# Kernel optimization log

Measured on AMD Instinct MI355X. Metric: run time of the kernel, lower is better.

Reference implementation:

```python
import jax, jax.numpy as jnp
import numpy as np

V, E, HID, T = 50000, 300, 256, 9
B, S = 32, 512
H = HID // 2  # per-direction LSTM hidden


def _lstm_dir(x, wih, whh, bih, bhh, reverse):
    # x: [B,S,D]; torch nn.LSTM gate order: i, f, g, o
    bsz = x.shape[0]
    hdim = whh.shape[1]
    xg = jnp.einsum('bsd,gd->bsg', x, wih) + bih + bhh  # [B,S,4H] precomputed input gates

    def step(carry, xt):
        h, c = carry
        g = xt + h @ whh.T
        i, f, gg, o = jnp.split(g, 4, axis=-1)
        c = jax.nn.sigmoid(f) * c + jax.nn.sigmoid(i) * jnp.tanh(gg)
        h = jax.nn.sigmoid(o) * jnp.tanh(c)
        return (h, c), h

    init = (jnp.zeros((bsz, hdim), x.dtype), jnp.zeros((bsz, hdim), x.dtype))
    _, hs = jax.lax.scan(step, init, jnp.swapaxes(xg, 0, 1), reverse=reverse)
    return jnp.swapaxes(hs, 0, 1)  # [B,S,H]


def _crf_nll(emissions, tags, mask, start_t, end_t, trans_t):
    # pytorch-crf: loss = -mean_b llh, llh = numerator - log-partition
    maskf = mask.astype(emissions.dtype)
    em_tag = jnp.take_along_axis(emissions, tags[..., None], axis=2)[..., 0]  # [B,S]
    trans_sc = trans_t[tags[:, :-1], tags[:, 1:]]  # [B,S-1]
    num = start_t[tags[:, 0]] + em_tag[:, 0] + jnp.sum((trans_sc + em_tag[:, 1:]) * maskf[:, 1:], axis=1)
    seq_len = mask.sum(axis=1)
    last_tags = jnp.take_along_axis(tags, (seq_len - 1)[:, None], axis=1)[:, 0]
    num = num + end_t[last_tags]

    def step(alpha, inp):
        em_t, m_t = inp  # [B,T], [B]
        new = jax.nn.logsumexp(alpha[:, :, None] + trans_t[None] + em_t[:, None, :], axis=1)
        return jnp.where(m_t[:, None], new, alpha), None

    alpha0 = start_t[None] + emissions[:, 0]
    alpha, _ = jax.lax.scan(step, alpha0, (jnp.swapaxes(emissions[:, 1:], 0, 1), jnp.swapaxes(mask[:, 1:], 0, 1)))
    denom = jax.nn.logsumexp(alpha + end_t[None], axis=1)
    return -(num - denom).mean()


def _forward(emb, wih0f, whh0f, bih0f, bhh0f, wih0b, whh0b, bih0b, bhh0b,
             wih1f, whh1f, bih1f, bhh1f, wih1b, whh1b, bih1b, bhh1b,
             wproj, bproj, start_t, end_t, trans_t, x, tags, mask):
    e = emb[x]  # [B,S,E]; dropout is identity in eval mode
    h0 = jnp.concatenate([_lstm_dir(e, wih0f, whh0f, bih0f, bhh0f, False),
                          _lstm_dir(e, wih0b, whh0b, bih0b, bhh0b, True)], axis=-1)
    h1 = jnp.concatenate([_lstm_dir(h0, wih1f, whh1f, bih1f, bhh1f, False),
                          _lstm_dir(h0, wih1b, whh1b, bih1b, bhh1b, True)], axis=-1)
    emissions = jnp.einsum('bsh,th->bst', h1, wproj) + bproj  # [B,S,T]
    return _crf_nll(emissions, tags, mask, start_t, end_t, trans_t)


def setup_inputs() -> dict:
    key = jax.random.key(0)
    ks = jax.random.split(key, 32)

    def n(k, shape, s=0.1):
        return jax.random.normal(k, shape, jnp.float32) * s

    d = {}
    d['emb'] = n(ks[0], (V, E)).at[0].set(0.0)  # padding_idx=0 row zeroed
    i = 1
    for l, din in enumerate([E, HID]):
        for dr in 'fb':
            d['wih%d%s' % (l, dr)] = n(ks[i], (4 * H, din)); i += 1
            d['whh%d%s' % (l, dr)] = n(ks[i], (4 * H, H)); i += 1
            d['bih%d%s' % (l, dr)] = n(ks[i], (4 * H,)); i += 1
            d['bhh%d%s' % (l, dr)] = n(ks[i], (4 * H,)); i += 1
    d['wproj'] = n(ks[i], (T, HID)); i += 1
    d['bproj'] = n(ks[i], (T,)); i += 1
    d['start_t'] = n(ks[i], (T,)); i += 1
    d['end_t'] = n(ks[i], (T,)); i += 1
    d['trans_t'] = n(ks[i], (T, T)); i += 1
    d['x'] = jax.random.randint(ks[i], (B, S), 1, V); i += 1
    d['tags'] = jax.random.randint(ks[i], (B, S), 0, T); i += 1
    d['mask'] = jnp.ones((B, S), bool)
    return d


def reference(emb, wih0f, whh0f, bih0f, bhh0f, wih0b, whh0b, bih0b, bhh0b,
              wih1f, whh1f, bih1f, bhh1f, wih1b, whh1b, bih1b, bhh1b,
              wproj, bproj, start_t, end_t, trans_t, x, tags, mask):
    return _forward(emb, wih0f, whh0f, bih0f, bhh0f, wih0b, whh0b, bih0b, bhh0b,
                    wih1f, whh1f, bih1f, bhh1f, wih1b, whh1b, bih1b, bhh1b,
                    wproj, bproj, start_t, end_t, trans_t, x, tags, mask)
```

## Files before the change

kernel.cpp:

```cpp
#include <hip/hip_runtime.h>
#include <hip/hip_bf16.h>

#define Vv 50000
#define Ee 300
#define HIDc 256
#define Tt 9
#define Bb 32
#define Ss 512
#define Hh 128
#define Mtok (Bb*Ss)

#define LSTM_NODOT2 0

__device__ __forceinline__ float sigm(float x) {
    return 1.0f / (1.0f + __expf(-x));
}
__device__ __forceinline__ float tanhx(float x) {
    return 1.0f - 2.0f / (__expf(2.0f * x) + 1.0f);
}

typedef _Float16 half2v __attribute__((ext_vector_type(2)));

__device__ __forceinline__ unsigned short f2h_bits(float x) {
    union { _Float16 h; unsigned short s; } u;
    u.h = (_Float16)x;
    return u.s;
}

__device__ __forceinline__ float dot2(unsigned int w, unsigned int h, float acc) {
    union { unsigned int u; half2v v; } a, b;
    a.u = w; b.u = h;
#if LSTM_NODOT2
    return acc + (float)a.v.x * (float)b.v.x + (float)a.v.y * (float)b.v.y;
#else
    return __builtin_amdgcn_fdot2(a.v, b.v, acc, false);
#endif
}

__global__ __launch_bounds__(256) void embed_gather(const float* __restrict__ emb,
                                                    const int* __restrict__ x,
                                                    float* __restrict__ e) {
    int idx = blockIdx.x * 256 + threadIdx.x;
    if (idx >= Mtok * 75) return;
    int token = idx / 75, q = idx % 75;
    ((float4*)e)[idx] = ((const float4*)emb)[(size_t)x[token] * 75 + q];
}

template<int K>
__global__ __launch_bounds__(256) void xg_gemm(const float* __restrict__ A,
                                               const float* __restrict__ Wf, const float* __restrict__ Wb,
                                               const float* __restrict__ bihf, const float* __restrict__ bhhf,
                                               const float* __restrict__ bihb, const float* __restrict__ bhhb,
                                               float* __restrict__ out) {
    constexpr int NKT = (K + 15) / 16;
    const int dir = blockIdx.z;
    const float* W   = dir ? Wb   : Wf;
    const float* bih = dir ? bihb : bihf;
    const float* bhh = dir ? bhhb : bhhf;
    const int m0 = blockIdx.y * 128;
    const int n0 = blockIdx.x * 64;

    __shared__ float As[16][128];
    __shared__ float Bs[16][64];

    const int tid = threadIdx.x;
    const int tx = tid & 15, ty = tid >> 4;
    const int ma = tid & 127, qa = tid >> 7;
    const int nw = tid & 63,  qw = tid >> 6;

    float acc[8][4] = {};

    for (int kt = 0; kt < NKT; ++kt) {
        const int k0 = kt * 16;
        #pragma unroll
        for (int r = 0; r < 2; ++r) {
            int kl = qa * 8 + r * 4;
            float4 v = make_float4(0.f, 0.f, 0.f, 0.f);
            if (k0 + kl < K)
                v = *(const float4*)(A + (size_t)(m0 + ma) * K + k0 + kl);
            As[kl + 0][ma] = v.x; As[kl + 1][ma] = v.y;
            As[kl + 2][ma] = v.z; As[kl + 3][ma] = v.w;
        }
        {
            int kl = qw * 4;
            float4 v = make_float4(0.f, 0.f, 0.f, 0.f);
            if (k0 + kl < K)
                v = *(const float4*)(W + (size_t)(n0 + nw) * K + k0 + kl);
            Bs[kl + 0][nw] = v.x; Bs[kl + 1][nw] = v.y;
            Bs[kl + 2][nw] = v.z; Bs[kl + 3][nw] = v.w;
        }
        __syncthreads();
        #pragma unroll
        for (int k = 0; k < 16; ++k) {
            float4 a0 = *(const float4*)&As[k][ty * 8];
            float4 a1 = *(const float4*)&As[k][ty * 8 + 4];
            float4 b  = *(const float4*)&Bs[k][tx * 4];
            float av[8] = {a0.x, a0.y, a0.z, a0.w, a1.x, a1.y, a1.z, a1.w};
            float bv[4] = {b.x, b.y, b.z, b.w};
            #pragma unroll
            for (int i = 0; i < 8; ++i)
                #pragma unroll
                for (int j = 0; j < 4; ++j)
                    acc[i][j] += av[i] * bv[j];
        }
        __syncthreads();
    }
    #pragma unroll
    for (int j = 0; j < 4; ++j) {
        int n = n0 + tx * 4 + j;
        float bsum = bih[n] + bhh[n];
        #pragma unroll
        for (int i = 0; i < 8; ++i) acc[i][j] += bsum;
    }
    #pragma unroll
    for (int i = 0; i < 8; ++i) {
        int m = m0 + ty * 8 + i;
        *(float4*)(out + ((size_t)dir * Mtok + m) * 512 + n0 + tx * 4) =
            make_float4(acc[i][0], acc[i][1], acc[i][2], acc[i][3]);
    }
}

__global__ __launch_bounds__(512, 1) void lstm_scan(const float* __restrict__ xg,
                                                    const float* __restrict__ whhf,
                                                    const float* __restrict__ whhb,
                                                    float* __restrict__ hout) {
    const int b   = blockIdx.x & 31;
    const int dir = blockIdx.x >> 5;
    const int tid = threadIdx.x;
    const int o   = tid;
    const float* whh = dir ? whhb : whhf;

    __shared__ unsigned short wlds16[16 * 512 * 8];
    __shared__ unsigned int   hp[64];
    __shared__ float          g_lds[512];

    for (int e = tid; e < 512 * 128; e += 512) {
        int ro = e >> 7, k = e & 127;
        wlds16[((k >> 3) * 512 + ro) * 8 + (k & 7)] = f2h_bits(whh[e]);
    }
    if (tid < 64) hp[tid] = 0u;
    float c = 0.f;
    __syncthreads();

    const float* xgb = xg + ((size_t)dir * Mtok + (size_t)b * Ss) * 512;
    int t = dir ? (Ss - 1) : 0;
    const int dt = dir ? -1 : 1;
    float xv = xgb[(size_t)t * 512 + o];
    const int cls = o >> 7;

    for (int step = 0; step < Ss; ++step) {
        float a0 = 0.f, a1 = 0.f, a2 = 0.f, a3 = 0.f;
        #pragma unroll
        for (int kc = 0; kc < 16; ++kc) {
            uint4 wv = *(const uint4*)(wlds16 + ((kc * 512 + o) * 8));
            uint4 hv = *(const uint4*)((const unsigned short*)hp + kc * 8);
            a0 = dot2(wv.x, hv.x, a0);
            a1 = dot2(wv.y, hv.y, a1);
            a2 = dot2(wv.z, hv.z, a2);
            a3 = dot2(wv.w, hv.w, a3);
        }
        float g = ((a0 + a1) + (a2 + a3)) + xv;
        int tn = t + dt;
        if (step + 1 < Ss) xv = xgb[(size_t)tn * 512 + o];
        g_lds[o] = (cls == 2) ? tanhx(g) : sigm(g);
        __syncthreads();
        if (tid < 128) {
            c = g_lds[tid + 128] * c + g_lds[tid] * g_lds[tid + 256];
            float h = g_lds[tid + 384] * tanhx(c);
            hout[((size_t)b * Ss + t) * 256 + dir * 128 + tid] = h;
            ((unsigned short*)hp)[tid] = f2h_bits(h);
        }
        __syncthreads();
        t = tn;
    }
}

__global__ __launch_bounds__(256) void emis_kernel(const float* __restrict__ h1,
                                                   const float* __restrict__ wproj,
                                                   const float* __restrict__ bproj,
                                                   float* __restrict__ em) {
    int idx = blockIdx.x * 256 + threadIdx.x;
    if (idx >= Mtok * Tt) return;
    int token = idx / Tt, tg = idx % Tt;
    const float4* hp = (const float4*)(h1 + (size_t)token * 256);
    const float4* wp = (const float4*)(wproj + (size_t)tg * 256);
    float acc = bproj[tg];
    #pragma unroll 8
    for (int q = 0; q < 64; ++q) {
        float4 a = hp[q], b = wp[q];
        acc += a.x * b.x + a.y * b.y + a.z * b.z + a.w * b.w;
    }
    em[idx] = acc;
}

__global__ __launch_bounds__(256) void crf_num(const float* __restrict__ em,
                                               const int* __restrict__ tags,
                                               const int* __restrict__ mask,
                                               const float* __restrict__ start_t,
                                               const float* __restrict__ end_t,
                                               const float* __restrict__ trans,
                                               float* __restrict__ num) {
    const int b = blockIdx.x;
    const int tid = threadIdx.x;
    __shared__ float sp[256];
    __shared__ int   sc[256];
    float p = 0.f; int cnt = 0;
    for (int t = 1 + tid; t < Ss; t += 256) {
        int mk = mask[b * Ss + t] != 0;
        int tg = tags[b * Ss + t], tp = tags[b * Ss + t - 1];
        if (mk) p += trans[tp * Tt + tg] + em[((size_t)b * Ss + t) * Tt + tg];
        cnt += mk;
    }
    if (tid == 0) cnt += (mask[b * Ss] != 0);
    sp[tid] = p; sc[tid] = cnt;
    __syncthreads();
    for (int s = 128; s > 0; s >>= 1) {
        if (tid < s) { sp[tid] += sp[tid + s]; sc[tid] += sc[tid + s]; }
        __syncthreads();
    }
    if (tid == 0) {
        int t0 = tags[b * Ss];
        float v = start_t[t0] + em[(size_t)b * Ss * Tt + t0] + sp[0];
        int sl = sc[0];
        v += end_t[tags[b * Ss + sl - 1]];
        num[b] = v;
    }
}

__global__ __launch_bounds__(512) void crf_alpha(const float* __restrict__ em,
                                                 const int* __restrict__ mask,
                                                 const float* __restrict__ start_t,
                                                 const float* __restrict__ end_t,
                                                 const float* __restrict__ trans,
                                                 const float* __restrict__ num,
                                                 float* __restrict__ out) {
    __shared__ float al[2][Bb][12];
    __shared__ float tr[Tt * Tt];
    __shared__ float red[Bb];
    const int tid = threadIdx.x;
    if (tid < Tt * Tt) tr[tid] = trans[tid];
    const int b = tid / Tt, j = tid % Tt;
    const bool act = tid < Bb * Tt;
    if (act) al[0][b][j] = start_t[j] + em[(size_t)b * Ss * Tt + j];
    __syncthreads();

    int cur = 0;
    float emn = act ? em[((size_t)b * Ss + 1) * Tt + j] : 0.f;
    for (int t = 1; t < Ss; ++t) {
        float nv = 0.f;
        if (act) {
            float v[Tt];
            float mx = -1e30f;
            #pragma unroll
            for (int i = 0; i < Tt; ++i) {
                v[i] = al[cur][b][i] + tr[i * Tt + j];
                mx = fmaxf(mx, v[i]);
            }
            float s = 0.f;
            #pragma unroll
            for (int i = 0; i < Tt; ++i) s += __expf(v[i] - mx);
            nv = mx + __logf(s) + emn;
            int mk = mask[b * Ss + t] != 0;
            if (t + 1 < Ss) emn = em[((size_t)b * Ss + t + 1) * Tt + j];
            if (!mk) nv = al[cur][b][j];
            al[cur ^ 1][b][j] = nv;
        }
        __syncthreads();
        cur ^= 1;
    }
    if (tid < Bb) {
        float mx = -1e30f;
        float v[Tt];
        #pragma unroll
        for (int jj = 0; jj < Tt; ++jj) {
            v[jj] = al[cur][tid][jj] + end_t[jj];
            mx = fmaxf(mx, v[jj]);
        }
        float s = 0.f;
        #pragma unroll
        for (int jj = 0; jj < Tt; ++jj) s += __expf(v[jj] - mx);
        float denom = mx + __logf(s);
        red[tid] = num[tid] - denom;
    }
    __syncthreads();
    if (tid == 0) {
        float s = 0.f;
        #pragma unroll
        for (int bb = 0; bb < Bb; ++bb) s += red[bb];
        out[0] = -(s / (float)Bb);
    }
}

extern "C" void kernel_launch(void* const* d_in, const int* in_sizes, int n_in,
                              void* d_out, int out_size, void* d_ws, size_t ws_size,
                              hipStream_t stream) {
    const float* emb   = (const float*)d_in[0];
    const float* wih0f = (const float*)d_in[1];  const float* whh0f = (const float*)d_in[2];
    const float* bih0f = (const float*)d_in[3];  const float* bhh0f = (const float*)d_in[4];
    const float* wih0b = (const float*)d_in[5];  const float* whh0b = (const float*)d_in[6];
    const float* bih0b = (const float*)d_in[7];  const float* bhh0b = (const float*)d_in[8];
    const float* wih1f = (const float*)d_in[9];  const float* whh1f = (const float*)d_in[10];
    const float* bih1f = (const float*)d_in[11]; const float* bhh1f = (const float*)d_in[12];
    const float* wih1b = (const float*)d_in[13]; const float* whh1b = (const float*)d_in[14];
    const float* bih1b = (const float*)d_in[15]; const float* bhh1b = (const float*)d_in[16];
    const float* wproj = (const float*)d_in[17]; const float* bproj = (const float*)d_in[18];
    const float* start_t = (const float*)d_in[19];
    const float* end_t   = (const float*)d_in[20];
    const float* trans_t = (const float*)d_in[21];
    const int* x    = (const int*)d_in[22];
    const int* tags = (const int*)d_in[23];
    const int* mask = (const int*)d_in[24];

    float* ws   = (float*)d_ws;
    float* e_buf = ws;
    float* xg    = e_buf + (size_t)Mtok * Ee;
    float* h0    = xg + (size_t)2 * Mtok * 512;
    float* em    = h0 + (size_t)Mtok * 256;
    float* num   = em + (size_t)Mtok * Tt;
    float* h1    = e_buf;
    float* outp  = (float*)d_out;

    embed_gather<<<(Mtok * 75 + 255) / 256, 256, 0, stream>>>(emb, x, e_buf);
    xg_gemm<Ee><<<dim3(8, 128, 2), 256, 0, stream>>>(e_buf, wih0f, wih0b,
                                                     bih0f, bhh0f, bih0b, bhh0b, xg);
    lstm_scan<<<64, 512, 0, stream>>>(xg, whh0f, whh0b, h0);
    xg_gemm<HIDc><<<dim3(8, 128, 2), 256, 0, stream>>>(h0, wih1f, wih1b,
                                                       bih1f, bhh1f, bih1b, bhh1b, xg);
    lstm_scan<<<64, 512, 0, stream>>>(xg, whh1f, whh1b, h1);
    emis_kernel<<<(Mtok * Tt + 255) / 256, 256, 0, stream>>>(h1, wproj, bproj, em);
    crf_num<<<32, 256, 0, stream>>>(em, tags, mask, start_t, end_t, trans_t, num);
    crf_alpha<<<1, 512, 0, stream>>>(em, mask, start_t, end_t, trans_t, num, outp);
}
```

Before: 1.468 ms.

## Keep LSTM recurrent weights resident in registers with two gate rows per thread

The recurrent scan block shrinks to 256 threads, each owning two gate rows. Each thread's fp16 W_hh slices are preloaded into registers once via inline ds_read_b128, so the per-step loop no longer reads weights from LDS. Only the shared hidden vector is read from LDS each step. This uses many more VGPRs and halves the thread count, which leaves fewer wavefronts to hide latency.

```diff
diff --git a/kernel.cpp b/kernel.cpp
--- a/kernel.cpp
+++ b/kernel.cpp
@@ -120,49 +120,71 @@
     }
 }
 
-__global__ __launch_bounds__(512, 1) void lstm_scan(const float* __restrict__ xg,
+#define W16(F) F(0) F(1) F(2) F(3) F(4) F(5) F(6) F(7) F(8) F(9) F(10) F(11) F(12) F(13) F(14) F(15)
+
+__global__ __launch_bounds__(256, 1) void lstm_scan(const float* __restrict__ xg,
                                                     const float* __restrict__ whhf,
                                                     const float* __restrict__ whhb,
                                                     float* __restrict__ hout) {
     const int b   = blockIdx.x & 31;
     const int dir = blockIdx.x >> 5;
     const int tid = threadIdx.x;
-    const int o   = tid;
     const float* whh = dir ? whhb : whhf;
 
     __shared__ unsigned short wlds16[16 * 512 * 8];
     __shared__ unsigned int   hp[64];
     __shared__ float          g_lds[512];
 
-    for (int e = tid; e < 512 * 128; e += 512) {
+    for (int e = tid; e < 512 * 128; e += 256) {
         int ro = e >> 7, k = e & 127;
         wlds16[((k >> 3) * 512 + ro) * 8 + (k & 7)] = f2h_bits(whh[e]);
     }
     if (tid < 64) hp[tid] = 0u;
+    __syncthreads();
+
+    const unsigned ldsbase = (unsigned)(size_t)wlds16;
+#define LDW(i) \
+    float4 wA##i; asm volatile("ds_read_b128 %0, %1" : "=v"(wA##i) \
+        : "v"(ldsbase + ((unsigned)(i) * 512u + (unsigned)tid) * 16u)); \
+    float4 wB##i; asm volatile("ds_read_b128 %0, %1" : "=v"(wB##i) \
+        : "v"(ldsbase + ((unsigned)(i) * 512u + (unsigned)tid + 256u) * 16u));
+    W16(LDW)
+#undef LDW
+    asm volatile("s_waitcnt lgkmcnt(0)");
+    __builtin_amdgcn_sched_barrier(0);
+
     float c = 0.f;
-    __syncthreads();
-
     const float* xgb = xg + ((size_t)dir * Mtok + (size_t)b * Ss) * 512;
     int t = dir ? (Ss - 1) : 0;
     const int dt = dir ? -1 : 1;
-    float xv = xgb[(size_t)t * 512 + o];
-    const int cls = o >> 7;
+    float xv0 = xgb[(size_t)t * 512 + tid];
+    float xv1 = xgb[(size_t)t * 512 + tid + 256];
+    const int cls1_tanh = (tid < 128);
 
     for (int step = 0; step < Ss; ++step) {
         float a0 = 0.f, a1 = 0.f, a2 = 0.f, a3 = 0.f;
-        #pragma unroll
-        for (int kc = 0; kc < 16; ++kc) {
-            uint4 wv = *(const uint4*)(wlds16 + ((kc * 512 + o) * 8));
-            uint4 hv = *(const uint4*)((const unsigned short*)hp + kc * 8);
-            a0 = dot2(wv.x, hv.x, a0);
-            a1 = dot2(wv.y, hv.y, a1);
-            a2 = dot2(wv.z, hv.z, a2);
-            a3 = dot2(wv.w, hv.w, a3);
-        }
-        float g = ((a0 + a1) + (a2 + a3)) + xv;
+        float b0 = 0.f, b1 = 0.f, b2 = 0.f, b3 = 0.f;
+#define DOTK(i) { \
+        uint4 hv = *(const uint4*)((const unsigned int*)hp + (i) * 4); \
+        a0 = dot2(__float_as_uint(wA##i.x), hv.x, a0); \
+        a1 = dot2(__float_as_uint(wA##i.y), hv.y, a1); \
+        a2 = dot2(__float_as_uint(wA##i.z), hv.z, a2); \
+        a3 = dot2(__float_as_uint(wA##i.w), hv.w, a3); \
+        b0 = dot2(__float_as_uint(wB##i.x), hv.x, b0); \
+        b1 = dot2(__float_as_uint(wB##i.y), hv.y, b1); \
+        b2 = dot2(__float_as_uint(wB##i.z), hv.z, b2); \
+        b3 = dot2(__float_as_uint(wB##i.w), hv.w, b3); }
+        W16(DOTK)
+#undef DOTK
+        float g0 = ((a0 + a1) + (a2 + a3)) + xv0;
+        float g1 = ((b0 + b1) + (b2 + b3)) + xv1;
         int tn = t + dt;
-        if (step + 1 < Ss) xv = xgb[(size_t)tn * 512 + o];
-        g_lds[o] = (cls == 2) ? tanhx(g) : sigm(g);
+        if (step + 1 < Ss) {
+            xv0 = xgb[(size_t)tn * 512 + tid];
+            xv1 = xgb[(size_t)tn * 512 + tid + 256];
+        }
+        g_lds[tid]       = sigm(g0);
+        g_lds[tid + 256] = cls1_tanh ? tanhx(g1) : sigm(g1);
         __syncthreads();
         if (tid < 128) {
             c = g_lds[tid + 128] * c + g_lds[tid] * g_lds[tid + 256];
@@ -323,10 +345,10 @@
     embed_gather<<<(Mtok * 75 + 255) / 256, 256, 0, stream>>>(emb, x, e_buf);
     xg_gemm<Ee><<<dim3(8, 128, 2), 256, 0, stream>>>(e_buf, wih0f, wih0b,
                                                      bih0f, bhh0f, bih0b, bhh0b, xg);
-    lstm_scan<<<64, 512, 0, stream>>>(xg, whh0f, whh0b, h0);
+    lstm_scan<<<64, 256, 0, stream>>>(xg, whh0f, whh0b, h0);
     xg_gemm<HIDc><<<dim3(8, 128, 2), 256, 0, stream>>>(h0, wih1f, wih1b,
                                                        bih1f, bhh1f, bih1b, bhh1b, xg);
-    lstm_scan<<<64, 512, 0, stream>>>(xg, whh1f, whh1b, h1);
+    lstm_scan<<<64, 256, 0, stream>>>(xg, whh1f, whh1b, h1);
     emis_kernel<<<(Mtok * Tt + 255) / 256, 256, 0, stream>>>(h1, wproj, bproj, em);
     crf_num<<<32, 256, 0, stream>>>(em, tags, mask, start_t, end_t, trans_t, num);
     crf_alpha<<<1, 512, 0, stream>>>(em, mask, start_t, end_t, trans_t, num, outp);
```

Result: slower. 1.517 ms (+3.4%).
